# Optimization experiments

Measured on AMD Instinct MI355X. Metric: run time of the kernel, lower is better.

Reference implementation:

```python
import jax, jax.numpy as jnp
import numpy as np

N_TOKENS = 8192
D_MODEL = 1024
HIDDEN = 4096   # d_model * expert_hidden_mult(4)
N_EXPERTS = 8
TOP_K = 2
LN_EPS = 1e-5


def setup_inputs() -> dict:
    key = jax.random.key(0)
    ks = jax.random.split(key, 8)
    s_in = 1.0 / np.sqrt(D_MODEL)
    s_h = 1.0 / np.sqrt(HIDDEN)
    return {
        "x": jax.random.normal(ks[0], (N_TOKENS, D_MODEL), jnp.float32),
        "Wr": jax.random.normal(ks[1], (D_MODEL, N_EXPERTS), jnp.float32) * s_in,
        "W1": jax.random.normal(ks[2], (N_EXPERTS, D_MODEL, HIDDEN), jnp.float32) * s_in,
        "b1": jnp.zeros((N_EXPERTS, HIDDEN), jnp.float32),
        "W2": jax.random.normal(ks[3], (N_EXPERTS, HIDDEN, D_MODEL), jnp.float32) * s_h,
        "b2": jnp.zeros((N_EXPERTS, D_MODEL), jnp.float32),
        "ln_w": jnp.ones((D_MODEL,), jnp.float32),
        "ln_b": jnp.zeros((D_MODEL,), jnp.float32),
    }


def reference(x, Wr, W1, b1, W2, b2, ln_w, ln_b):
    N, d = x.shape
    E = Wr.shape[1]
    # --- Router: top-k softmax gates scattered into dense [N, E] ---
    logits = x @ Wr                                   # [N, E]
    topv, topi = jax.lax.top_k(logits, TOP_K)         # [N, K]
    gv = jax.nn.softmax(topv, axis=-1)                # renormalized top-k gates
    gates = jnp.zeros_like(logits).at[jnp.arange(N)[:, None], topi].set(gv)
    # --- Experts: gate_e > 0 masks tokens; zero gate contributes zero, so
    # dense per-expert FFN weighted by the (mostly-zero) gate column is the
    # same math as the original gather/FFN/scatter-add dispatch. ---
    mixed = jnp.zeros_like(x)
    for e in range(E):  # small fixed expert count
        h = jax.nn.gelu(x @ W1[e] + b1[e])            # [N, HIDDEN]
        y = h @ W2[e] + b2[e]                         # [N, d]
        mixed = mixed + gates[:, e:e + 1] * y
    # --- Load-balancing aux loss (importance * load) ---
    importance = jnp.mean(jax.nn.softmax(logits, axis=-1), axis=0)  # [E]
    load = jnp.mean((gates > 0).astype(x.dtype), axis=0)            # [E]
    aux_loss = E * jnp.sum(importance * load)
    # --- Residual + LayerNorm (output_dropout is identity in eval) ---
    res = x + mixed
    mu = jnp.mean(res, axis=-1, keepdims=True)
    var = jnp.var(res, axis=-1, keepdims=True)
    out = (res - mu) * jax.lax.rsqrt(var + LN_EPS) * ln_w + ln_b
    return out, aux_loss
```

## Files before the change

### kernel.cpp

```cpp
#include <hip/hip_runtime.h>

#define N_TOK 8192
#define DM 1024
#define HID 4096
#define NE 8
#define MAX_TILES 136
#define MAX_SLOTS (MAX_TILES * 128)
#define LN_EPS 1e-5f

typedef __attribute__((ext_vector_type(8))) _Float16 f16x8;
typedef __attribute__((ext_vector_type(4))) _Float16 f16x4;
typedef __attribute__((ext_vector_type(4))) float f32x4;

constexpr size_t OFF_WT1 = 0;
constexpr size_t OFF_WT2 = OFF_WT1 + (size_t)NE * HID * DM * 2;
constexpr size_t OFF_XG  = OFF_WT2 + (size_t)NE * DM * HID * 2;
constexpr size_t OFF_H   = OFF_XG + (size_t)MAX_SLOTS * DM * 2;
constexpr size_t OFF_Y   = OFF_H + (size_t)MAX_SLOTS * HID * 2;
constexpr size_t OFF_TOPI = OFF_Y + (size_t)MAX_SLOTS * DM * 2;
constexpr size_t OFF_TOPG = OFF_TOPI + (size_t)N_TOK * 2 * 4;
constexpr size_t OFF_PTOK = OFF_TOPG + (size_t)N_TOK * 2 * 4;
constexpr size_t OFF_SLOT = OFF_PTOK + (size_t)MAX_SLOTS * 4;
constexpr size_t OFF_HDR = OFF_SLOT + (size_t)N_TOK * 2 * 4;
constexpr size_t WS_NEEDED = OFF_HDR + 4096;

__device__ inline float gelu_fast(float v) {
  float c = 0.7978845608028654f * (v + 0.044715f * v * v * v);
  return v / (1.0f + __expf(-2.0f * c));
}

__device__ inline void g2l16(const _Float16* g, _Float16* l) {
  __builtin_amdgcn_global_load_lds(
      (const __attribute__((address_space(1))) unsigned int*)g,
      (__attribute__((address_space(3))) unsigned int*)l, 16, 0, 0);
}

__device__ inline int swz32(int row, int c) {
  return c ^ ((row + (row >> 2)) & 3);
}

__global__ __launch_bounds__(256) void k_router(
    const float* __restrict__ x, const float* __restrict__ Wr,
    int* __restrict__ topi, float* __restrict__ topg,
    int* __restrict__ cnt, float* __restrict__ imp) {
  __shared__ float wr[NE * DM];
  __shared__ float blkImp[NE];
  __shared__ int blkCnt[NE];
  int tid = threadIdx.x;
  if (tid < NE) { blkImp[tid] = 0.0f; blkCnt[tid] = 0; }
  for (int i = tid; i < DM * NE; i += 256)
    wr[(i & 7) * DM + (i >> 3)] = Wr[i];
  __syncthreads();
  int wave = tid >> 6, lane = tid & 63;
  for (int it = 0; it < 4; ++it) {
    int t = blockIdx.x * 16 + wave * 4 + it;
    double acc[NE];
#pragma unroll
    for (int e = 0; e < NE; ++e) acc[e] = 0.0;
    for (int j = 0; j < DM / 256; ++j) {
      int d = j * 256 + lane * 4;
      float4 xv = *(const float4*)(x + (size_t)t * DM + d);
#pragma unroll
      for (int e = 0; e < NE; ++e) {
        float4 wv = *(const float4*)(wr + e * DM + d);
        acc[e] += (double)xv.x * wv.x + (double)xv.y * wv.y +
                  (double)xv.z * wv.z + (double)xv.w * wv.w;
      }
    }
#pragma unroll
    for (int off = 32; off > 0; off >>= 1) {
#pragma unroll
      for (int e = 0; e < NE; ++e) acc[e] += __shfl_down(acc[e], off);
    }
    if (lane == 0) {
      int i0 = 0;
#pragma unroll
      for (int e = 1; e < NE; ++e) if (acc[e] > acc[i0]) i0 = e;
      int i1 = (i0 == 0) ? 1 : 0;
#pragma unroll
      for (int e = 0; e < NE; ++e) if (e != i0 && acc[e] > acc[i1]) i1 = e;
      double g0 = 1.0 / (1.0 + exp(acc[i1] - acc[i0]));
      topi[t * 2] = i0; topi[t * 2 + 1] = i1;
      topg[t * 2] = (float)g0; topg[t * 2 + 1] = (float)(1.0 - g0);
      atomicAdd(&blkCnt[i0], 1); atomicAdd(&blkCnt[i1], 1);
      double mx = acc[0];
#pragma unroll
      for (int e = 1; e < NE; ++e) mx = acc[e] > mx ? acc[e] : mx;
      double s = 0.0, p[NE];
#pragma unroll
      for (int e = 0; e < NE; ++e) { p[e] = exp(acc[e] - mx); s += p[e]; }
      double inv = 1.0 / s;
#pragma unroll
      for (int e = 0; e < NE; ++e) atomicAdd(&blkImp[e], (float)(p[e] * inv));
    }
  }
  __syncthreads();
  if (tid < NE) { atomicAdd(&cnt[tid], blkCnt[tid]); atomicAdd(&imp[tid], blkImp[tid]); }
}

__global__ void k_setup(int* __restrict__ hdr, float* __restrict__ aux_out) {
  int* cnt = hdr;
  float* imp = (float*)(hdr + 8);
  int* cursor = hdr + 16;
  int* off = hdr + 24;
  int* n_tiles_p = hdr + 33;
  int* tile_expert = hdr + 34;
  if (threadIdx.x == 0) {
    int offl[NE + 1];
    int o = 0;
    for (int e = 0; e < NE; ++e) {
      offl[e] = o; off[e] = o; cursor[e] = o;
      o += ((cnt[e] + 127) >> 7) << 7;
    }
    offl[NE] = o; off[NE] = o;
    int nt = o >> 7;
    *n_tiles_p = nt;
    int e = 0;
    for (int i = 0; i < nt; ++i) {
      while (i * 128 >= offl[e + 1]) ++e;
      tile_expert[i] = e;
    }
    double a = 0.0;
    for (int e2 = 0; e2 < NE; ++e2)
      a += ((double)imp[e2] / (double)N_TOK) * ((double)cnt[e2] / (double)N_TOK);
    *aux_out = (float)((double)NE * a);
  }
}

__global__ __launch_bounds__(256) void k_init_pairs(int* __restrict__ pair_token) {
  int i = blockIdx.x * 256 + threadIdx.x;
  if (i < MAX_SLOTS) pair_token[i] = -1;
}

__global__ __launch_bounds__(256) void k_scatter(
    const int* __restrict__ topi, int* __restrict__ cursor,
    int* __restrict__ pair_token, int* __restrict__ slot_of) {
  int t = blockIdx.x * 256 + threadIdx.x;
#pragma unroll
  for (int k = 0; k < 2; ++k) {
    int e = topi[t * 2 + k];
    int p = atomicAdd(&cursor[e], 1);
    pair_token[p] = t;
    slot_of[t * 2 + k] = p;
  }
}

__global__ __launch_bounds__(256) void k_gather(
    const float* __restrict__ x, const int* __restrict__ pair_token,
    _Float16* __restrict__ Xg) {
  int slot = blockIdx.x;
  int t = pair_token[slot];
  int d = threadIdx.x * 4;
  f16x4 v4 = {0, 0, 0, 0};
  if (t >= 0) {
    float4 v = *(const float4*)(x + (size_t)t * DM + d);
    v4[0] = (_Float16)v.x; v4[1] = (_Float16)v.y;
    v4[2] = (_Float16)v.z; v4[3] = (_Float16)v.w;
  }
  *(f16x4*)(Xg + (size_t)slot * DM + d) = v4;
}

__global__ __launch_bounds__(256) void k_transpose(
    const float* __restrict__ in, _Float16* __restrict__ out, int R, int C) {
  __shared__ float t[64 * 65];
  size_t base = (size_t)blockIdx.z * R * C;
  int c0 = blockIdx.x * 64, r0 = blockIdx.y * 64;
  int cx = (threadIdx.x & 15) * 4, ry = threadIdx.x >> 4;
#pragma unroll
  for (int p = 0; p < 4; ++p) {
    int r = p * 16 + ry;
    float4 v = *(const float4*)(in + base + (size_t)(r0 + r) * C + c0 + cx);
    t[r * 65 + cx] = v.x; t[r * 65 + cx + 1] = v.y;
    t[r * 65 + cx + 2] = v.z; t[r * 65 + cx + 3] = v.w;
  }
  __syncthreads();
#pragma unroll
  for (int q = 0; q < 2; ++q) {
    int lin = q * 256 + threadIdx.x;
    int c = lin >> 3, ch = lin & 7;
    f16x8 v;
#pragma unroll
    for (int j = 0; j < 8; ++j) v[j] = (_Float16)t[(ch * 8 + j) * 65 + c];
    *(f16x8*)(out + base + (size_t)(c0 + c) * R + r0 + ch * 8) = v;
  }
}

template <int KD, int ND, bool GELU>
__global__ __launch_bounds__(256, 2) void k_ffn(
    const _Float16* __restrict__ A, const _Float16* __restrict__ Bw,
    const float* __restrict__ bias, _Float16* __restrict__ C,
    const int* __restrict__ hdr) {
  constexpr int GX = ND / 256;
  constexpr int NWG = GX * MAX_TILES;
  constexpr int Q = NWG >> 3;
  constexpr int R = NWG & 7;
  constexpr int NSTEP = KD / 32;
  constexpr int BUF = 384 * 32;
  int orig = blockIdx.y * GX + blockIdx.x;
  int xcd = orig & 7, loc = orig >> 3;
  int wg = (xcd < R ? xcd * (Q + 1) : R * (Q + 1) + (xcd - R) * Q) + loc;
  int tileM = wg / GX, tileN = wg % GX;
  if (tileM >= hdr[33]) return;
  int e = hdr[34 + tileM];
  __shared__ _Float16 lds[2 * BUF];
  int tid = threadIdx.x;
  int wave = tid >> 6, lane = tid & 63;
  int l16 = lane & 15, quad = lane >> 4;
  int wbase = tid & 192;
  const _Float16* Ag = A + (size_t)tileM * 128 * KD;
  const _Float16* Bg = Bw + (size_t)e * ND * KD + (size_t)tileN * 256 * KD;

  const _Float16* ga0; const _Float16* ga1;
  const _Float16* gb0; const _Float16* gb1; const _Float16* gb2; const _Float16* gb3;
  {
    int s, r;
    s = tid;        r = s >> 2; ga0 = Ag + (size_t)r * KD + swz32(r, s & 3) * 8;
    s = 256 + tid;  r = s >> 2; ga1 = Ag + (size_t)r * KD + swz32(r, s & 3) * 8;
    s = tid;        r = s >> 2; gb0 = Bg + (size_t)r * KD + swz32(r, s & 3) * 8;
    s = 256 + tid;  r = s >> 2; gb1 = Bg + (size_t)r * KD + swz32(r, s & 3) * 8;
    s = 512 + tid;  r = s >> 2; gb2 = Bg + (size_t)r * KD + swz32(r, s & 3) * 8;
    s = 768 + tid;  r = s >> 2; gb3 = Bg + (size_t)r * KD + swz32(r, s & 3) * 8;
  }
  int aoff[8], boff[4];
#pragma unroll
  for (int mi = 0; mi < 8; ++mi) {
    int r = mi * 16 + l16;
    aoff[mi] = r * 32 + (swz32(r, quad) << 3);
  }
#pragma unroll
  for (int ni = 0; ni < 4; ++ni) {
    int r = wave * 64 + ni * 16 + l16;
    boff[ni] = 128 * 32 + r * 32 + (swz32(r, quad) << 3);
  }

  f32x4 acc[8][4];
  const f32x4 fz = {0.f, 0.f, 0.f, 0.f};
#pragma unroll
  for (int a = 0; a < 8; ++a)
#pragma unroll
    for (int b = 0; b < 4; ++b) acc[a][b] = fz;

  auto stage = [&](int t, _Float16* buf) {
    int k = t * 32;
    g2l16(ga0 + k, buf + (size_t)(0 * 256 + wbase) * 8);
    g2l16(ga1 + k, buf + (size_t)(1 * 256 + wbase) * 8);
    _Float16* bb = buf + 128 * 32;
    g2l16(gb0 + k, bb + (size_t)(0 * 256 + wbase) * 8);
    g2l16(gb1 + k, bb + (size_t)(1 * 256 + wbase) * 8);
    g2l16(gb2 + k, bb + (size_t)(2 * 256 + wbase) * 8);
    g2l16(gb3 + k, bb + (size_t)(3 * 256 + wbase) * 8);
  };
  auto compute = [&](const _Float16* buf) {
    f16x8 af[8], bf[4];
#pragma unroll
    for (int mi = 0; mi < 8; ++mi) af[mi] = *(const f16x8*)(buf + aoff[mi]);
#pragma unroll
    for (int ni = 0; ni < 4; ++ni) bf[ni] = *(const f16x8*)(buf + boff[ni]);
#pragma unroll
    for (int mi = 0; mi < 8; ++mi)
#pragma unroll
      for (int ni = 0; ni < 4; ++ni)
        acc[mi][ni] = __builtin_amdgcn_mfma_f32_16x16x32_f16(af[mi], bf[ni], acc[mi][ni], 0, 0, 0);
  };

  stage(0, lds);
  __syncthreads();
#pragma unroll 1
  for (int t = 0; t < NSTEP; t += 2) {
    stage(t + 1, lds + BUF);
    compute(lds);
    __syncthreads();
    if (t + 2 < NSTEP) stage(t + 2, lds);
    compute(lds + BUF);
    __syncthreads();
  }

  int rowBase = tileM * 128;
  int colBase = tileN * 256 + wave * 64;
  _Float16* sc = lds + wave * 4096;
  float bv[4];
#pragma unroll
  for (int ni = 0; ni < 4; ++ni) bv[ni] = bias[e * ND + colBase + ni * 16 + l16];
#pragma unroll
  for (int h = 0; h < 2; ++h) {
#pragma unroll
    for (int mi = 0; mi < 4; ++mi)
#pragma unroll
      for (int ni = 0; ni < 4; ++ni)
#pragma unroll
        for (int i = 0; i < 4; ++i) {
          int rr = mi * 16 + quad * 4 + i;
          int c2 = ni * 16 + l16;
          float v = acc[h * 4 + mi][ni][i] + bv[ni];
          sc[rr * 64 + c2] = (_Float16)(GELU ? gelu_fast(v) : v);
        }
    __syncthreads();
#pragma unroll
    for (int j = 0; j < 8; ++j) {
      int lin = j * 64 + lane;
      int rr = lin >> 3, ch = lin & 7;
      f16x8 v = *(const f16x8*)(sc + rr * 64 + ch * 8);
      *(f16x8*)(C + (size_t)(rowBase + h * 64 + rr) * ND + colBase + ch * 8) = v;
    }
    __syncthreads();
  }
}

__global__ __launch_bounds__(256) void k_ln(
    const float* __restrict__ x, const _Float16* __restrict__ Y,
    const int* __restrict__ slot_of, const float* __restrict__ topg,
    const float* __restrict__ lnw, const float* __restrict__ lnb,
    float* __restrict__ out) {
  int t = blockIdx.x, tid = threadIdx.x;
  int s0 = slot_of[t * 2], s1 = slot_of[t * 2 + 1];
  float g0 = topg[t * 2], g1 = topg[t * 2 + 1];
  float4 xv = ((const float4*)(x + (size_t)t * DM))[tid];
  f16x4 y0 = ((const f16x4*)(Y + (size_t)s0 * DM))[tid];
  f16x4 y1 = ((const f16x4*)(Y + (size_t)s1 * DM))[tid];
  float r0 = xv.x + g0 * (float)y0[0] + g1 * (float)y1[0];
  float r1 = xv.y + g0 * (float)y0[1] + g1 * (float)y1[1];
  float r2 = xv.z + g0 * (float)y0[2] + g1 * (float)y1[2];
  float r3 = xv.w + g0 * (float)y0[3] + g1 * (float)y1[3];
  float s = r0 + r1 + r2 + r3;
  float s2 = r0 * r0 + r1 * r1 + r2 * r2 + r3 * r3;
#pragma unroll
  for (int off = 32; off > 0; off >>= 1) {
    s += __shfl_down(s, off);
    s2 += __shfl_down(s2, off);
  }
  __shared__ float ss[4], ss2[4];
  int wave = tid >> 6, lane = tid & 63;
  if (lane == 0) { ss[wave] = s; ss2[wave] = s2; }
  __syncthreads();
  float S = ss[0] + ss[1] + ss[2] + ss[3];
  float S2 = ss2[0] + ss2[1] + ss2[2] + ss2[3];
  float mu = S * (1.0f / DM);
  float var = S2 * (1.0f / DM) - mu * mu;
  float inv = rsqrtf(var + LN_EPS);
  float4 wv = ((const float4*)lnw)[tid];
  float4 bv = ((const float4*)lnb)[tid];
  float4 o;
  o.x = (r0 - mu) * inv * wv.x + bv.x;
  o.y = (r1 - mu) * inv * wv.y + bv.y;
  o.z = (r2 - mu) * inv * wv.z + bv.z;
  o.w = (r3 - mu) * inv * wv.w + bv.w;
  ((float4*)(out + (size_t)t * DM))[tid] = o;
}

__global__ void k_sentinel(float* out, float v) { out[threadIdx.x] = v; }

extern "C" void kernel_launch(void* const* d_in, const int* in_sizes, int n_in,
                              void* d_out, int out_size, void* d_ws, size_t ws_size,
                              hipStream_t stream) {
  const float* x = (const float*)d_in[0];
  const float* Wr = (const float*)d_in[1];
  const float* W1 = (const float*)d_in[2];
  const float* b1 = (const float*)d_in[3];
  const float* W2 = (const float*)d_in[4];
  const float* b2 = (const float*)d_in[5];
  const float* lnw = (const float*)d_in[6];
  const float* lnb = (const float*)d_in[7];
  float* out = (float*)d_out;
  char* ws = (char*)d_ws;

  if (ws_size < WS_NEEDED) {
    k_sentinel<<<1, 256, 0, stream>>>(out, 1.0e6f + (float)(ws_size >> 20));
    return;
  }

  _Float16* Wt1 = (_Float16*)(ws + OFF_WT1);
  _Float16* Wt2 = (_Float16*)(ws + OFF_WT2);
  _Float16* Xg = (_Float16*)(ws + OFF_XG);
  _Float16* Hbuf = (_Float16*)(ws + OFF_H);
  _Float16* Ybuf = (_Float16*)(ws + OFF_Y);
  int* topi = (int*)(ws + OFF_TOPI);
  float* topg = (float*)(ws + OFF_TOPG);
  int* pair_token = (int*)(ws + OFF_PTOK);
  int* slot_of = (int*)(ws + OFF_SLOT);
  int* hdr = (int*)(ws + OFF_HDR);
  int* cnt = hdr;
  float* imp = (float*)(hdr + 8);
  int* cursor = hdr + 16;

  hipMemsetAsync(hdr, 0, 64, stream);

  k_transpose<<<dim3(HID / 64, DM / 64, NE), 256, 0, stream>>>(W1, Wt1, DM, HID);
  k_transpose<<<dim3(DM / 64, HID / 64, NE), 256, 0, stream>>>(W2, Wt2, HID, DM);
  k_router<<<512, 256, 0, stream>>>(x, Wr, topi, topg, cnt, imp);
  k_setup<<<1, 1, 0, stream>>>(hdr, out + (size_t)N_TOK * DM);
  k_init_pairs<<<(MAX_SLOTS + 255) / 256, 256, 0, stream>>>(pair_token);
  k_scatter<<<N_TOK / 256, 256, 0, stream>>>(topi, cursor, pair_token, slot_of);
  k_gather<<<MAX_SLOTS, 256, 0, stream>>>(x, pair_token, Xg);
  k_ffn<DM, HID, true><<<dim3(HID / 256, MAX_TILES), 256, 0, stream>>>(Xg, Wt1, b1, Hbuf, hdr);
  k_ffn<HID, DM, false><<<dim3(DM / 256, MAX_TILES), 256, 0, stream>>>(Hbuf, Wt2, b2, Ybuf, hdr);
  k_ln<<<N_TOK, 256, 0, stream>>>(x, Ybuf, slot_of, topg, lnw, lnb, out);
}
```

Measured before the change: 899.9 us.

## Use 256x256 GEMM tiles, 4-stage LDS pipeline, split-K for second FFN

```diff
diff --git a/kernel.cpp b/kernel.cpp
--- a/kernel.cpp
+++ b/kernel.cpp
@@ -4,7 +4,7 @@
 #define DM 1024
 #define HID 4096
 #define NE 8
-#define MAX_TILES 136
+#define MAX_TILES 144
 #define MAX_SLOTS (MAX_TILES * 128)
 #define LN_EPS 1e-5f
 
@@ -16,12 +16,13 @@
 constexpr size_t OFF_WT2 = OFF_WT1 + (size_t)NE * HID * DM * 2;
 constexpr size_t OFF_XG  = OFF_WT2 + (size_t)NE * DM * HID * 2;
 constexpr size_t OFF_H   = OFF_XG + (size_t)MAX_SLOTS * DM * 2;
-constexpr size_t OFF_Y   = OFF_H + (size_t)MAX_SLOTS * HID * 2;
-constexpr size_t OFF_TOPI = OFF_Y + (size_t)MAX_SLOTS * DM * 2;
+constexpr size_t OFF_TOPI = OFF_H + (size_t)MAX_SLOTS * HID * 2;
 constexpr size_t OFF_TOPG = OFF_TOPI + (size_t)N_TOK * 2 * 4;
 constexpr size_t OFF_PTOK = OFF_TOPG + (size_t)N_TOK * 2 * 4;
 constexpr size_t OFF_SLOT = OFF_PTOK + (size_t)MAX_SLOTS * 4;
 constexpr size_t OFF_HDR = OFF_SLOT + (size_t)N_TOK * 2 * 4;
+constexpr size_t OFF_Y  = OFF_WT1;
+constexpr size_t OFF_Y1 = OFF_XG;
 constexpr size_t WS_NEEDED = OFF_HDR + 4096;
 
 __device__ inline float gelu_fast(float v) {
@@ -35,8 +36,16 @@
       (__attribute__((address_space(3))) unsigned int*)l, 16, 0, 0);
 }
 
-__device__ inline int swz32(int row, int c) {
-  return c ^ ((row + (row >> 2)) & 3);
+__device__ inline void stage32(const _Float16* __restrict__ g, int ld,
+                               _Float16* __restrict__ part, int tid) {
+#pragma unroll
+  for (int p = 0; p < 2; ++p) {
+    int s = p * 512 + tid;
+    int vr = s >> 3;
+    int c7 = (s & 7) ^ (vr & 7);
+    g2l16(g + (size_t)(2 * vr + (c7 >> 2)) * ld + (c7 & 3) * 8,
+          part + (size_t)(p * 512 + (tid & 448)) * 8);
+  }
 }
 
 __global__ __launch_bounds__(256) void k_router(
@@ -110,7 +119,7 @@
     int o = 0;
     for (int e = 0; e < NE; ++e) {
       offl[e] = o; off[e] = o; cursor[e] = o;
-      o += ((cnt[e] + 127) >> 7) << 7;
+      o += ((cnt[e] + 255) >> 8) << 8;
     }
     offl[NE] = o; off[NE] = o;
     int nt = o >> 7;
@@ -185,52 +194,43 @@
   }
 }
 
-template <int KD, int ND, bool GELU>
-__global__ __launch_bounds__(256, 2) void k_ffn(
+template <int KD, int LDK, int ND, bool GELU>
+__global__ __launch_bounds__(512, 2) void k_ffn(
     const _Float16* __restrict__ A, const _Float16* __restrict__ Bw,
-    const float* __restrict__ bias, _Float16* __restrict__ C,
-    const int* __restrict__ hdr) {
+    const float* __restrict__ bias, _Float16* __restrict__ C0,
+    _Float16* __restrict__ C1, const int* __restrict__ hdr) {
   constexpr int GX = ND / 256;
-  constexpr int NWG = GX * MAX_TILES;
-  constexpr int Q = NWG >> 3;
-  constexpr int R = NWG & 7;
-  constexpr int NSTEP = KD / 32;
-  constexpr int BUF = 384 * 32;
+  constexpr int NWG = GX * (MAX_TILES / 2);
+  constexpr int Q = NWG >> 3, R = NWG & 7;
+  constexpr int NST = KD / 32;
+  constexpr int SLOT = 256 * 64;
   int orig = blockIdx.y * GX + blockIdx.x;
   int xcd = orig & 7, loc = orig >> 3;
   int wg = (xcd < R ? xcd * (Q + 1) : R * (Q + 1) + (xcd - R) * Q) + loc;
   int tileM = wg / GX, tileN = wg % GX;
-  if (tileM >= hdr[33]) return;
-  int e = hdr[34 + tileM];
-  __shared__ _Float16 lds[2 * BUF];
+  if (tileM * 2 >= hdr[33]) return;
+  int e = hdr[34 + tileM * 2];
+  __shared__ _Float16 lds[4 * SLOT];
   int tid = threadIdx.x;
   int wave = tid >> 6, lane = tid & 63;
+  int wm = wave >> 2, wn = wave & 3;
   int l16 = lane & 15, quad = lane >> 4;
-  int wbase = tid & 192;
-  const _Float16* Ag = A + (size_t)tileM * 128 * KD;
-  const _Float16* Bg = Bw + (size_t)e * ND * KD + (size_t)tileN * 256 * KD;
-
-  const _Float16* ga0; const _Float16* ga1;
-  const _Float16* gb0; const _Float16* gb1; const _Float16* gb2; const _Float16* gb3;
-  {
-    int s, r;
-    s = tid;        r = s >> 2; ga0 = Ag + (size_t)r * KD + swz32(r, s & 3) * 8;
-    s = 256 + tid;  r = s >> 2; ga1 = Ag + (size_t)r * KD + swz32(r, s & 3) * 8;
-    s = tid;        r = s >> 2; gb0 = Bg + (size_t)r * KD + swz32(r, s & 3) * 8;
-    s = 256 + tid;  r = s >> 2; gb1 = Bg + (size_t)r * KD + swz32(r, s & 3) * 8;
-    s = 512 + tid;  r = s >> 2; gb2 = Bg + (size_t)r * KD + swz32(r, s & 3) * 8;
-    s = 768 + tid;  r = s >> 2; gb3 = Bg + (size_t)r * KD + swz32(r, s & 3) * 8;
-  }
+  const _Float16* Ag = A + (size_t)tileM * 256 * LDK + (size_t)blockIdx.z * KD;
+  const _Float16* Bg = Bw + (size_t)e * ND * LDK + (size_t)tileN * 256 * LDK +
+                       (size_t)blockIdx.z * KD;
+
   int aoff[8], boff[4];
 #pragma unroll
   for (int mi = 0; mi < 8; ++mi) {
-    int r = mi * 16 + l16;
-    aoff[mi] = r * 32 + (swz32(r, quad) << 3);
+    int r = wm * 128 + mi * 16 + l16;
+    int v = r >> 1, c = ((r & 1) << 2) | quad;
+    aoff[mi] = v * 64 + ((c ^ (v & 7)) << 3);
   }
 #pragma unroll
   for (int ni = 0; ni < 4; ++ni) {
-    int r = wave * 64 + ni * 16 + l16;
-    boff[ni] = 128 * 32 + r * 32 + (swz32(r, quad) << 3);
+    int r = wn * 64 + ni * 16 + l16;
+    int v = r >> 1, c = ((r & 1) << 2) | quad;
+    boff[ni] = 8192 + v * 64 + ((c ^ (v & 7)) << 3);
   }
 
   f32x4 acc[8][4];
@@ -240,47 +240,53 @@
 #pragma unroll
     for (int b = 0; b < 4; ++b) acc[a][b] = fz;
 
-  auto stage = [&](int t, _Float16* buf) {
-    int k = t * 32;
-    g2l16(ga0 + k, buf + (size_t)(0 * 256 + wbase) * 8);
-    g2l16(ga1 + k, buf + (size_t)(1 * 256 + wbase) * 8);
-    _Float16* bb = buf + 128 * 32;
-    g2l16(gb0 + k, bb + (size_t)(0 * 256 + wbase) * 8);
-    g2l16(gb1 + k, bb + (size_t)(1 * 256 + wbase) * 8);
-    g2l16(gb2 + k, bb + (size_t)(2 * 256 + wbase) * 8);
-    g2l16(gb3 + k, bb + (size_t)(3 * 256 + wbase) * 8);
-  };
-  auto compute = [&](const _Float16* buf) {
+#pragma unroll
+  for (int jj = 0; jj < 3; ++jj) {
+    stage32(Ag + jj * 32, LDK, lds + jj * SLOT, tid);
+    stage32(Bg + jj * 32, LDK, lds + jj * SLOT + 8192, tid);
+  }
+  asm volatile("s_waitcnt vmcnt(8)" ::: "memory");
+  __builtin_amdgcn_s_barrier();
+
+#pragma unroll 1
+  for (int j = 0; j < NST; ++j) {
+    __builtin_amdgcn_sched_barrier(0);
+    const _Float16* sl = lds + (j & 3) * SLOT;
     f16x8 af[8], bf[4];
 #pragma unroll
-    for (int mi = 0; mi < 8; ++mi) af[mi] = *(const f16x8*)(buf + aoff[mi]);
-#pragma unroll
-    for (int ni = 0; ni < 4; ++ni) bf[ni] = *(const f16x8*)(buf + boff[ni]);
+    for (int mi = 0; mi < 8; ++mi) af[mi] = *(const f16x8*)(sl + aoff[mi]);
+#pragma unroll
+    for (int ni = 0; ni < 4; ++ni) bf[ni] = *(const f16x8*)(sl + boff[ni]);
+    if (j + 3 < NST) {
+      _Float16* dst = lds + ((j + 3) & 3) * SLOT;
+      stage32(Ag + (j + 3) * 32, LDK, dst, tid);
+      stage32(Bg + (j + 3) * 32, LDK, dst + 8192, tid);
+    }
+    __builtin_amdgcn_s_setprio(1);
 #pragma unroll
     for (int mi = 0; mi < 8; ++mi)
 #pragma unroll
       for (int ni = 0; ni < 4; ++ni)
         acc[mi][ni] = __builtin_amdgcn_mfma_f32_16x16x32_f16(af[mi], bf[ni], acc[mi][ni], 0, 0, 0);
-  };
-
-  stage(0, lds);
-  __syncthreads();
-#pragma unroll 1
-  for (int t = 0; t < NSTEP; t += 2) {
-    stage(t + 1, lds + BUF);
-    compute(lds);
-    __syncthreads();
-    if (t + 2 < NSTEP) stage(t + 2, lds);
-    compute(lds + BUF);
-    __syncthreads();
-  }
-
-  int rowBase = tileM * 128;
-  int colBase = tileN * 256 + wave * 64;
+    __builtin_amdgcn_s_setprio(0);
+    asm volatile("s_waitcnt lgkmcnt(0)" ::: "memory");
+    __builtin_amdgcn_sched_barrier(0);
+    if (j < NST - 3)       asm volatile("s_waitcnt vmcnt(8)" ::: "memory");
+    else if (j == NST - 3) asm volatile("s_waitcnt vmcnt(4)" ::: "memory");
+    else                   asm volatile("s_waitcnt vmcnt(0)" ::: "memory");
+    __builtin_amdgcn_sched_barrier(0);
+    __builtin_amdgcn_s_barrier();
+  }
+
+  int rowBase = tileM * 256 + wm * 128;
+  int colBase = tileN * 256 + wn * 64;
+  _Float16* Cout = blockIdx.z ? C1 : C0;
+  float bscale = blockIdx.z ? 0.f : 1.f;
   _Float16* sc = lds + wave * 4096;
   float bv[4];
 #pragma unroll
-  for (int ni = 0; ni < 4; ++ni) bv[ni] = bias[e * ND + colBase + ni * 16 + l16];
+  for (int ni = 0; ni < 4; ++ni)
+    bv[ni] = bscale * bias[e * ND + colBase + ni * 16 + l16];
 #pragma unroll
   for (int h = 0; h < 2; ++h) {
 #pragma unroll
@@ -296,11 +302,11 @@
         }
     __syncthreads();
 #pragma unroll
-    for (int j = 0; j < 8; ++j) {
-      int lin = j * 64 + lane;
+    for (int jj = 0; jj < 8; ++jj) {
+      int lin = jj * 64 + lane;
       int rr = lin >> 3, ch = lin & 7;
       f16x8 v = *(const f16x8*)(sc + rr * 64 + ch * 8);
-      *(f16x8*)(C + (size_t)(rowBase + h * 64 + rr) * ND + colBase + ch * 8) = v;
+      *(f16x8*)(Cout + (size_t)(rowBase + h * 64 + rr) * ND + colBase + ch * 8) = v;
     }
     __syncthreads();
   }
@@ -308,6 +314,7 @@
 
 __global__ __launch_bounds__(256) void k_ln(
     const float* __restrict__ x, const _Float16* __restrict__ Y,
+    const _Float16* __restrict__ Y1,
     const int* __restrict__ slot_of, const float* __restrict__ topg,
     const float* __restrict__ lnw, const float* __restrict__ lnb,
     float* __restrict__ out) {
@@ -317,10 +324,16 @@
   float4 xv = ((const float4*)(x + (size_t)t * DM))[tid];
   f16x4 y0 = ((const f16x4*)(Y + (size_t)s0 * DM))[tid];
   f16x4 y1 = ((const f16x4*)(Y + (size_t)s1 * DM))[tid];
-  float r0 = xv.x + g0 * (float)y0[0] + g1 * (float)y1[0];
-  float r1 = xv.y + g0 * (float)y0[1] + g1 * (float)y1[1];
-  float r2 = xv.z + g0 * (float)y0[2] + g1 * (float)y1[2];
-  float r3 = xv.w + g0 * (float)y0[3] + g1 * (float)y1[3];
+  f16x4 z0 = ((const f16x4*)(Y1 + (size_t)s0 * DM))[tid];
+  f16x4 z1 = ((const f16x4*)(Y1 + (size_t)s1 * DM))[tid];
+  float a0 = (float)y0[0] + (float)z0[0], a1 = (float)y0[1] + (float)z0[1];
+  float a2 = (float)y0[2] + (float)z0[2], a3 = (float)y0[3] + (float)z0[3];
+  float b0 = (float)y1[0] + (float)z1[0], b1v = (float)y1[1] + (float)z1[1];
+  float b2v = (float)y1[2] + (float)z1[2], b3 = (float)y1[3] + (float)z1[3];
+  float r0 = xv.x + g0 * a0 + g1 * b0;
+  float r1 = xv.y + g0 * a1 + g1 * b1v;
+  float r2 = xv.z + g0 * a2 + g1 * b2v;
+  float r3 = xv.w + g0 * a3 + g1 * b3;
   float s = r0 + r1 + r2 + r3;
   float s2 = r0 * r0 + r1 * r1 + r2 * r2 + r3 * r3;
 #pragma unroll
@@ -373,6 +386,7 @@
   _Float16* Xg = (_Float16*)(ws + OFF_XG);
   _Float16* Hbuf = (_Float16*)(ws + OFF_H);
   _Float16* Ybuf = (_Float16*)(ws + OFF_Y);
+  _Float16* Ybuf1 = (_Float16*)(ws + OFF_Y1);
   int* topi = (int*)(ws + OFF_TOPI);
   float* topg = (float*)(ws + OFF_TOPG);
   int* pair_token = (int*)(ws + OFF_PTOK);
@@ -391,7 +405,9 @@
   k_init_pairs<<<(MAX_SLOTS + 255) / 256, 256, 0, stream>>>(pair_token);
   k_scatter<<<N_TOK / 256, 256, 0, stream>>>(topi, cursor, pair_token, slot_of);
   k_gather<<<MAX_SLOTS, 256, 0, stream>>>(x, pair_token, Xg);
-  k_ffn<DM, HID, true><<<dim3(HID / 256, MAX_TILES), 256, 0, stream>>>(Xg, Wt1, b1, Hbuf, hdr);
-  k_ffn<HID, DM, false><<<dim3(DM / 256, MAX_TILES), 256, 0, stream>>>(Hbuf, Wt2, b2, Ybuf, hdr);
-  k_ln<<<N_TOK, 256, 0, stream>>>(x, Ybuf, slot_of, topg, lnw, lnb, out);
-}
+  k_ffn<DM, DM, HID, true><<<dim3(HID / 256, MAX_TILES / 2, 1), 512, 0, stream>>>(
+      Xg, Wt1, b1, Hbuf, Hbuf, hdr);
+  k_ffn<HID / 2, HID, DM, false><<<dim3(DM / 256, MAX_TILES / 2, 2), 512, 0, stream>>>(
+      Hbuf, Wt2, b2, Ybuf, Ybuf1, hdr);
+  k_ln<<<N_TOK, 256, 0, stream>>>(x, Ybuf, Ybuf1, slot_of, topg, lnw, lnb, out);
+}
```

Measured after the change: 906.9 us. About the same (+0.8%).
